# Kernel optimization log

Measured on AMD Instinct MI355X. Metric: run time of the kernel, lower is better.

The kernel has to match this reference:

```python
import jax, jax.numpy as jnp
import numpy as np

B, SEQ, D, H, PRED = 131072, 150, 2, 64, 150


def setup_inputs() -> dict:
    key = jax.random.key(0)
    ks = jax.random.split(key, 5)
    s1 = 1.0 / np.sqrt(D)  # torch Linear default init bounds
    s2 = 1.0 / np.sqrt(H)
    return {
        "x": jax.random.normal(ks[0], (B, SEQ, D), jnp.float32),
        "W1": jax.random.uniform(ks[1], (D, H), jnp.float32, -s1, s1),
        "b1": jax.random.uniform(ks[2], (H,), jnp.float32, -s1, s1),
        "W2": jax.random.uniform(ks[3], (H, D), jnp.float32, -s2, s2),
        "b2": jax.random.uniform(ks[4], (D,), jnp.float32, -s2, s2),
    }


def reference(x, W1, b1, W2, b2):
    # ODE RHS: autonomous 2-layer MLP, f(t, y) = tanh(y W1 + b1) W2 + b2
    def f(y):
        return jnp.tanh(y @ W1 + b1) @ W2 + b2

    y0 = x[:, -1, :]  # [B, D]
    t = jnp.linspace(0.0, float(PRED), PRED)  # 150 grid points -> 149 steps
    dts = t[1:] - t[:-1]  # each = 150/149

    # torchdiffeq method='rk4' uses the 3/8-rule fixed-grid step (rk4_alt_step_func)
    def step(y, dt):
        k1 = f(y)
        k2 = f(y + dt * k1 / 3.0)
        k3 = f(y + dt * (k2 - k1 / 3.0))
        k4 = f(y + dt * (k1 - k2 + k3))
        y1 = y + dt * (k1 + 3.0 * (k2 + k3) + k4) / 8.0
        return y1, y1

    _, ys = jax.lax.scan(step, y0, dts)  # ys: [PRED-1, B, D]
    pred = jnp.concatenate([y0[None], ys], axis=0)  # [PRED, B, D]
    return pred.transpose(1, 0, 2)  # [B, PRED, D]
```

## Files before the change

### kernel.cpp

```cpp
#include <hip/hip_runtime.h>

#ifndef __has_builtin
#define __has_builtin(x) 0
#endif

__device__ __forceinline__ float fast_exp2(float x) {
#if __has_builtin(__builtin_amdgcn_exp2f)
  return __builtin_amdgcn_exp2f(x);
#else
  return exp2f(x);
#endif
}
__device__ __forceinline__ float fast_rcp(float x) {
#if __has_builtin(__builtin_amdgcn_rcpf)
  return __builtin_amdgcn_rcpf(x);
#else
  return 1.0f / x;
#endif
}

namespace {
constexpr int kB = 131072;
constexpr int kSeq = 150;
constexpr int kD = 2;
constexpr int kH = 64;
constexpr int kPred = 150;
constexpr int kSteps = kPred - 1;
constexpr float kDt = 150.0f / 149.0f;
constexpr float kC = 2.8853900817779268f;
}

__device__ __forceinline__ void feval(float y0, float y1,
                                      const float4* __restrict__ sw,
                                      const float4* __restrict__ sb4,
                                      float base0, float base1,
                                      float& f0, float& f1) {
  float a0 = 0.0f, a1 = 0.0f, c0 = 0.0f, c1 = 0.0f;
#pragma unroll 4
  for (int q = 0; q < kH / 4; ++q) {
    float4 bb = sb4[q];
    float4 w0 = sw[4 * q + 0];
    float p0 = fmaf(y0, w0.x, fmaf(y1, w0.y, bb.x));
    float r0 = fast_rcp(1.0f + fast_exp2(p0));
    a0 = fmaf(r0, w0.z, a0);
    a1 = fmaf(r0, w0.w, a1);
    float4 w1 = sw[4 * q + 1];
    float p1 = fmaf(y0, w1.x, fmaf(y1, w1.y, bb.y));
    float r1 = fast_rcp(1.0f + fast_exp2(p1));
    c0 = fmaf(r1, w1.z, c0);
    c1 = fmaf(r1, w1.w, c1);
    float4 w2 = sw[4 * q + 2];
    float p2 = fmaf(y0, w2.x, fmaf(y1, w2.y, bb.z));
    float r2 = fast_rcp(1.0f + fast_exp2(p2));
    a0 = fmaf(r2, w2.z, a0);
    a1 = fmaf(r2, w2.w, a1);
    float4 w3 = sw[4 * q + 3];
    float p3 = fmaf(y0, w3.x, fmaf(y1, w3.y, bb.w));
    float r3 = fast_rcp(1.0f + fast_exp2(p3));
    c0 = fmaf(r3, w3.z, c0);
    c1 = fmaf(r3, w3.w, c1);
  }
  f0 = base0 + a0 + c0;
  f1 = base1 + a1 + c1;
}

__global__ __launch_bounds__(256, 2) void ode_kernel(
    const float* __restrict__ x, const float* __restrict__ W1,
    const float* __restrict__ b1, const float* __restrict__ W2,
    const float* __restrict__ b2, float* __restrict__ out) {
  __shared__ float4 sw[kH];
  __shared__ float4 sb4[kH / 4];
  __shared__ float sbase[2];

  const int t = threadIdx.x;
  if (t < kH) {
    sw[t] = make_float4(W1[t] * kC, W1[kH + t] * kC,
                        -2.0f * W2[2 * t], -2.0f * W2[2 * t + 1]);
    reinterpret_cast<float*>(sb4)[t] = b1[t] * kC;
  }
  if (t < 2) {
    float s = b2[t];
    for (int j = 0; j < kH; ++j) s += W2[2 * j + t];
    sbase[t] = s;
  }
  __syncthreads();
  const float base0 = sbase[0], base1 = sbase[1];

  const long bidx = (long)blockIdx.x * blockDim.x + t;
  const float* xp = x + bidx * (long)(kSeq * kD) + (kSeq - 1) * kD;
  float y0 = xp[0];
  float y1 = xp[1];
  float* op = out + bidx * (long)(kPred * kD);

  float py0 = y0, py1 = y1;
  constexpr float DT = kDt, DT3 = kDt / 3.0f, DT8 = kDt / 8.0f;

  for (int s = 1; s <= kSteps; ++s) {
    float k1x, k1y, k2x, k2y, k3x, k3y, k4x, k4y;
    feval(y0, y1, sw, sb4, base0, base1, k1x, k1y);
    feval(fmaf(DT3, k1x, y0), fmaf(DT3, k1y, y1), sw, sb4, base0, base1, k2x, k2y);
    feval(fmaf(DT, k2x, fmaf(-DT3, k1x, y0)),
          fmaf(DT, k2y, fmaf(-DT3, k1y, y1)), sw, sb4, base0, base1, k3x, k3y);
    feval(fmaf(DT, k1x - k2x + k3x, y0),
          fmaf(DT, k1y - k2y + k3y, y1), sw, sb4, base0, base1, k4x, k4y);
    y0 = fmaf(DT8, k1x + 3.0f * (k2x + k3x) + k4x, y0);
    y1 = fmaf(DT8, k1y + 3.0f * (k2y + k3y) + k4y, y1);

    if (s & 1) {
      float4 v = make_float4(py0, py1, y0, y1);
      *reinterpret_cast<float4*>(op + (long)(s - 1) * 2) = v;
    } else {
      py0 = y0;
      py1 = y1;
    }
  }
}

extern "C" void kernel_launch(void* const* d_in, const int* in_sizes, int n_in,
                              void* d_out, int out_size, void* d_ws,
                              size_t ws_size, hipStream_t stream) {
  const float* x = (const float*)d_in[0];
  const float* W1 = (const float*)d_in[1];
  const float* b1 = (const float*)d_in[2];
  const float* W2 = (const float*)d_in[3];
  const float* b2 = (const float*)d_in[4];
  float* out = (float*)d_out;

  dim3 grid(kB / 256);
  dim3 block(256);
  hipLaunchKernelGGL(ode_kernel, grid, block, 0, stream, x, W1, b1, W2, b2,
                     out);
}
```

Measured before the change: 1.421 ms.

## Pack MLP FMAs into v2f ops and skip transcendentals when wave saturated

Splits the shared-memory weight layout into separate float4 arrays (W1 x/y columns, bias, W2 columns) so pairs of hidden units can use packed two-wide FMAs. Adds a wave-uniform check: when all four hidden preactivations in a group are large in magnitude for every lane, the sigmoid is replaced by a 0/1 step, skipping exp2 and rcp. This targets the transcendental and FMA instruction count in the inner MLP loop. The branch adds compare and ballot overhead, and the saturation shortcut introduces a small approximation error near the threshold.

```diff
diff --git a/kernel.cpp b/kernel.cpp
--- a/kernel.cpp
+++ b/kernel.cpp
@@ -3,6 +3,8 @@
 #ifndef __has_builtin
 #define __has_builtin(x) 0
 #endif
+
+typedef float v2f __attribute__((ext_vector_type(2)));
 
 __device__ __forceinline__ float fast_exp2(float x) {
 #if __has_builtin(__builtin_amdgcn_exp2f)
@@ -18,6 +20,9 @@
   return 1.0f / x;
 #endif
 }
+__device__ __forceinline__ v2f pk_fma(v2f a, v2f b, v2f c) {
+  return __builtin_elementwise_fma(a, b, c);
+}
 
 namespace {
 constexpr int kB = 131072;
@@ -28,55 +33,67 @@
 constexpr int kSteps = kPred - 1;
 constexpr float kDt = 150.0f / 149.0f;
 constexpr float kC = 2.8853900817779268f;
+constexpr float kSatP = 24.25f;
 }
 
-__device__ __forceinline__ void feval(float y0, float y1,
-                                      const float4* __restrict__ sw,
-                                      const float4* __restrict__ sb4,
-                                      float base0, float base1,
-                                      float& f0, float& f1) {
-  float a0 = 0.0f, a1 = 0.0f, c0 = 0.0f, c1 = 0.0f;
+__device__ __forceinline__ void feval(
+    float y0, float y1, const float4* __restrict__ swx,
+    const float4* __restrict__ swy, const float4* __restrict__ sbb,
+    const float4* __restrict__ swz, const float4* __restrict__ sww,
+    float base0, float base1, float& f0, float& f1) {
+  const v2f y0v = {y0, y0}, y1v = {y1, y1};
+  v2f a0 = {0.f, 0.f}, a1 = {0.f, 0.f};
+  v2f c0 = {0.f, 0.f}, c1 = {0.f, 0.f};
 #pragma unroll 4
-  for (int q = 0; q < kH / 4; ++q) {
-    float4 bb = sb4[q];
-    float4 w0 = sw[4 * q + 0];
-    float p0 = fmaf(y0, w0.x, fmaf(y1, w0.y, bb.x));
-    float r0 = fast_rcp(1.0f + fast_exp2(p0));
-    a0 = fmaf(r0, w0.z, a0);
-    a1 = fmaf(r0, w0.w, a1);
-    float4 w1 = sw[4 * q + 1];
-    float p1 = fmaf(y0, w1.x, fmaf(y1, w1.y, bb.y));
-    float r1 = fast_rcp(1.0f + fast_exp2(p1));
-    c0 = fmaf(r1, w1.z, c0);
-    c1 = fmaf(r1, w1.w, c1);
-    float4 w2 = sw[4 * q + 2];
-    float p2 = fmaf(y0, w2.x, fmaf(y1, w2.y, bb.z));
-    float r2 = fast_rcp(1.0f + fast_exp2(p2));
-    a0 = fmaf(r2, w2.z, a0);
-    a1 = fmaf(r2, w2.w, a1);
-    float4 w3 = sw[4 * q + 3];
-    float p3 = fmaf(y0, w3.x, fmaf(y1, w3.y, bb.w));
-    float r3 = fast_rcp(1.0f + fast_exp2(p3));
-    c0 = fmaf(r3, w3.z, c0);
-    c1 = fmaf(r3, w3.w, c1);
+  for (int g = 0; g < kH / 4; ++g) {
+    const float4 wx = swx[g], wy = swy[g], bb = sbb[g];
+    const float4 wz = swz[g], ww = sww[g];
+    v2f p01 = pk_fma(y0v, (v2f){wx.x, wx.y},
+                     pk_fma(y1v, (v2f){wy.x, wy.y}, (v2f){bb.x, bb.y}));
+    v2f p23 = pk_fma(y0v, (v2f){wx.z, wx.w},
+                     pk_fma(y1v, (v2f){wy.z, wy.w}, (v2f){bb.z, bb.w}));
+    float m = fminf(fminf(fabsf(p01.x), fabsf(p01.y)),
+                    fminf(fabsf(p23.x), fabsf(p23.y)));
+    v2f r01, r23;
+    if (__all(m > kSatP)) {
+      r01.x = p01.x < 0.f ? 1.f : 0.f;
+      r01.y = p01.y < 0.f ? 1.f : 0.f;
+      r23.x = p23.x < 0.f ? 1.f : 0.f;
+      r23.y = p23.y < 0.f ? 1.f : 0.f;
+    } else {
+      v2f t01 = {fast_exp2(p01.x), fast_exp2(p01.y)};
+      v2f t23 = {fast_exp2(p23.x), fast_exp2(p23.y)};
+      t01 = t01 + (v2f){1.f, 1.f};
+      t23 = t23 + (v2f){1.f, 1.f};
+      r01.x = fast_rcp(t01.x);
+      r01.y = fast_rcp(t01.y);
+      r23.x = fast_rcp(t23.x);
+      r23.y = fast_rcp(t23.y);
+    }
+    a0 = pk_fma(r01, (v2f){wz.x, wz.y}, a0);
+    c0 = pk_fma(r23, (v2f){wz.z, wz.w}, c0);
+    a1 = pk_fma(r01, (v2f){ww.x, ww.y}, a1);
+    c1 = pk_fma(r23, (v2f){ww.z, ww.w}, c1);
   }
-  f0 = base0 + a0 + c0;
-  f1 = base1 + a1 + c1;
+  f0 = base0 + ((a0.x + a0.y) + (c0.x + c0.y));
+  f1 = base1 + ((a1.x + a1.y) + (c1.x + c1.y));
 }
 
 __global__ __launch_bounds__(256, 2) void ode_kernel(
     const float* __restrict__ x, const float* __restrict__ W1,
     const float* __restrict__ b1, const float* __restrict__ W2,
     const float* __restrict__ b2, float* __restrict__ out) {
-  __shared__ float4 sw[kH];
-  __shared__ float4 sb4[kH / 4];
+  __shared__ float4 swx[kH / 4], swy[kH / 4], sbb[kH / 4];
+  __shared__ float4 swz[kH / 4], sww[kH / 4];
   __shared__ float sbase[2];
 
   const int t = threadIdx.x;
   if (t < kH) {
-    sw[t] = make_float4(W1[t] * kC, W1[kH + t] * kC,
-                        -2.0f * W2[2 * t], -2.0f * W2[2 * t + 1]);
-    reinterpret_cast<float*>(sb4)[t] = b1[t] * kC;
+    reinterpret_cast<float*>(swx)[t] = W1[t] * kC;
+    reinterpret_cast<float*>(swy)[t] = W1[kH + t] * kC;
+    reinterpret_cast<float*>(sbb)[t] = b1[t] * kC;
+    reinterpret_cast<float*>(swz)[t] = -2.0f * W2[2 * t];
+    reinterpret_cast<float*>(sww)[t] = -2.0f * W2[2 * t + 1];
   }
   if (t < 2) {
     float s = b2[t];
@@ -97,12 +114,14 @@
 
   for (int s = 1; s <= kSteps; ++s) {
     float k1x, k1y, k2x, k2y, k3x, k3y, k4x, k4y;
-    feval(y0, y1, sw, sb4, base0, base1, k1x, k1y);
-    feval(fmaf(DT3, k1x, y0), fmaf(DT3, k1y, y1), sw, sb4, base0, base1, k2x, k2y);
+    feval(y0, y1, swx, swy, sbb, swz, sww, base0, base1, k1x, k1y);
+    feval(fmaf(DT3, k1x, y0), fmaf(DT3, k1y, y1), swx, swy, sbb, swz, sww,
+          base0, base1, k2x, k2y);
     feval(fmaf(DT, k2x, fmaf(-DT3, k1x, y0)),
-          fmaf(DT, k2y, fmaf(-DT3, k1y, y1)), sw, sb4, base0, base1, k3x, k3y);
-    feval(fmaf(DT, k1x - k2x + k3x, y0),
-          fmaf(DT, k1y - k2y + k3y, y1), sw, sb4, base0, base1, k4x, k4y);
+          fmaf(DT, k2y, fmaf(-DT3, k1y, y1)), swx, swy, sbb, swz, sww, base0,
+          base1, k3x, k3y);
+    feval(fmaf(DT, k1x - k2x + k3x, y0), fmaf(DT, k1y - k2y + k3y, y1), swx,
+          swy, sbb, swz, sww, base0, base1, k4x, k4y);
     y0 = fmaf(DT8, k1x + 3.0f * (k2x + k3x) + k4x, y0);
     y1 = fmaf(DT8, k1y + 3.0f * (k2y + k3y) + k4y, y1);
 
```

Measured after the change: 1.706 ms. 1.2x slower.
